# Kernel tuning notes

Measured on AMD Instinct MI355X. Metric: run time of the kernel, lower is better.

Reference implementation:

```python
import jax, jax.numpy as jnp
import numpy as np

N, E, D, C = 100000, 200000, 32, 8
H = 2 * C * C          # 128, MLP hidden
OUT = 4 * C * C + 4 * C  # 288, MLP output


def setup_inputs() -> dict:
    key = jax.random.key(0)
    ks = jax.random.split(key, 10)
    return {
        "x": jax.random.normal(ks[0], (N, D, C), jnp.float32),
        "edge_index": jax.random.randint(ks[1], (2, E), 0, N, jnp.int64),
        "edge_features_a": jax.random.normal(ks[2], (E, D, C), jnp.float32),
        "edge_features_b": jax.random.normal(ks[3], (E, D, C), jnp.float32),
        "edge_matrices": jax.random.normal(ks[4], (E, D, D), jnp.float32),
        "W1": jax.random.normal(ks[5], (H, H), jnp.float32) / np.sqrt(H),
        "b1": jnp.zeros((H,), jnp.float32),
        "ln_g": jnp.ones((H,), jnp.float32),
        "ln_b": jnp.zeros((H,), jnp.float32),
        "W2": jax.random.normal(ks[6], (H, OUT), jnp.float32) / np.sqrt(H),
        "b2": jnp.zeros((OUT,), jnp.float32),
    }


def _matrix_norm(w):
    # unit Frobenius norm over last two dims (MatrixNormalization, scale=1)
    n = jnp.sqrt(jnp.sum(w * w, axis=(-2, -1), keepdims=True))
    return w / (n + 1e-6)


def reference(x, edge_index, edge_features_a, edge_features_b, edge_matrices,
              W1, b1, ln_g, ln_b, W2, b2):
    c = x.shape[-1]
    x_node_a = x[edge_index[0]]                     # [E, D, C]
    x_node_b = x[edge_index[1]]                     # [E, D, C]

    edge_overlap = jnp.einsum('eij,eic,ejm->ecm', edge_matrices,
                              edge_features_a, edge_features_b)  # [E, C, C]
    node_overlap = jnp.einsum('eij,eic,ejm->ecm', edge_matrices,
                              x_node_a, x_node_b)                # [E, C, C]

    h = jnp.concatenate([edge_overlap.reshape(edge_overlap.shape[0], -1),
                         node_overlap.reshape(node_overlap.shape[0], -1)], axis=-1)
    h = jax.nn.silu(h @ W1 + b1)
    mu = jnp.mean(h, axis=-1, keepdims=True)
    var = jnp.var(h, axis=-1, keepdims=True)
    h = (h - mu) / jnp.sqrt(var + 1e-5) * ln_g + ln_b
    mlp_res = h @ W2 + b2                           # [E, 4C^2 + 4C]

    weights = mlp_res[:, :4 * c * c]
    factors = mlp_res[:, 4 * c * c:]
    ew_a, ew_b, nw_a, nw_b = jnp.split(weights, 4, axis=-1)
    ew_a = _matrix_norm(ew_a.reshape(-1, c, c))
    ew_b = _matrix_norm(ew_b.reshape(-1, c, c))
    nw_a = _matrix_norm(nw_a.reshape(-1, c, c))
    nw_b = _matrix_norm(nw_b.reshape(-1, c, c))

    f_ea = factors[:, None, 0 * c:1 * c]
    f_eb = factors[:, None, 1 * c:2 * c]
    f_na = factors[:, None, 2 * c:3 * c]
    f_nb = factors[:, None, 3 * c:4 * c]

    x_edge_a = (f_ea * (edge_features_a @ ew_a) + f_na * (x_node_a @ nw_a)) / 2
    x_edge_b = (f_eb * (edge_features_b @ ew_b) + f_nb * (x_node_b @ nw_b)) / 2
    return (x_edge_a, x_edge_b)
```

## Files before the change

### kernel.cpp

```cpp
#include <hip/hip_runtime.h>
#include <hip/hip_fp16.h>

typedef _Float16 f16;
typedef _Float16 half8 __attribute__((ext_vector_type(8)));
typedef _Float16 half4 __attribute__((ext_vector_type(4)));
typedef float f32x4 __attribute__((ext_vector_type(4)));

static __device__ __forceinline__ void fence_lds(){
  asm volatile("s_waitcnt lgkmcnt(0)" ::: "memory");
  __builtin_amdgcn_sched_barrier(0);
}

__global__ void k0_convert(const float* __restrict__ W1, const float* __restrict__ W2,
                           f16* __restrict__ W1T, f16* __restrict__ W2T){
  int o = blockIdx.x*256 + threadIdx.x;
  if (o < 128*128){
    int j = o >> 7, i = o & 127;
    W1T[o] = (f16)W1[i*128 + j];
  } else {
    int o2 = o - 128*128;
    int n = o2 >> 7, i = o2 & 127;
    W2T[o2] = (f16)W2[i*288 + n];
  }
}

struct ERegs { f32x4 a, b, xa, xb, m0, m1, m2, m3; };

static __device__ __forceinline__ ERegs load_edge(
    const float* __restrict__ x, const int* __restrict__ eidx,
    const float* __restrict__ efa, const float* __restrict__ efb,
    const float* __restrict__ em, int e, int E, int l){
  ERegs r;
  const size_t eb = (size_t)e * 256;
  const int ia = eidx[e], ib = eidx[E + e];
  r.a  = *(const f32x4*)(efa + eb + l*4);
  r.b  = *(const f32x4*)(efb + eb + l*4);
  r.xa = *(const f32x4*)(x + (size_t)ia*256 + l*4);
  r.xb = *(const f32x4*)(x + (size_t)ib*256 + l*4);
  const size_t mb = (size_t)e * 1024;
  r.m0 = *(const f32x4*)(em + mb +   0 + l*4);
  r.m1 = *(const f32x4*)(em + mb + 256 + l*4);
  r.m2 = *(const f32x4*)(em + mb + 512 + l*4);
  r.m3 = *(const f32x4*)(em + mb + 768 + l*4);
  return r;
}

__global__ __launch_bounds__(256, 3) void k_fused(
    const float* __restrict__ x, const int* __restrict__ eidx,
    const float* __restrict__ efa, const float* __restrict__ efb,
    const float* __restrict__ em,
    const f16* __restrict__ W1T, const f16* __restrict__ W2T,
    const float* __restrict__ b1, const float* __restrict__ lng,
    const float* __restrict__ lnb, const float* __restrict__ b2,
    float* __restrict__ outA, float* outB, int E)
{
  __shared__ f16 sWk[17024];

  const int tid = threadIdx.x;
  const int l = tid & 63, w = tid >> 6, q = l >> 4, n16 = l & 15;
  const int e0 = blockIdx.x * 16;

  f16*   sH0   = sWk + 12800;
  f16*   sH1   = sWk + 9344;
  float* sStat = (float*)sWk;
  float* sR    = (float*)sWk;

  f16* Mb   = sWk + w*3200;
  f16* AXT  = Mb + 1280;
  f16* BXT  = AXT + 640;
  f16* MBXT = BXT + 640;

  half4 hA[4], hXa[4], hB[4], hXb[4];

  ERegs cur = load_edge(x, eidx, efa, efb, em, e0 + w*4, E, l);
  #pragma unroll
  for (int i = 0; i < 4; ++i){
    const int le = w*4 + i;
    ERegs nxt;
    if (i < 3) nxt = load_edge(x, eidx, efa, efb, em, e0 + le + 1, E, l);

    {
      int d = l >> 1, cb = (l & 1)*4;
      half4 ta, txa, tb, txb;
      #pragma unroll
      for (int j = 0; j < 4; ++j){
        int c = cb + j;
        f16 va  = (f16)cur.a[j],  vxa = (f16)cur.xa[j];
        f16 vb  = (f16)cur.b[j],  vxb = (f16)cur.xb[j];
        AXT[c*40 + d]     = va;   AXT[(8+c)*40 + d] = vxa;
        BXT[c*40 + d]     = vb;   BXT[(8+c)*40 + d] = vxb;
        ta[j] = va; txa[j] = vxa; tb[j] = vb; txb[j] = vxb;
      }
      hA[i] = ta; hXa[i] = txa; hB[i] = tb; hXb[i] = txb;
      int r0 = l >> 3, c0 = (l & 7)*4;
      f16* p0 = Mb + ( 0 + r0)*40 + c0;
      p0[0]=(f16)cur.m0[0]; p0[1]=(f16)cur.m0[1]; p0[2]=(f16)cur.m0[2]; p0[3]=(f16)cur.m0[3];
      f16* p1 = Mb + ( 8 + r0)*40 + c0;
      p1[0]=(f16)cur.m1[0]; p1[1]=(f16)cur.m1[1]; p1[2]=(f16)cur.m1[2]; p1[3]=(f16)cur.m1[3];
      f16* p2 = Mb + (16 + r0)*40 + c0;
      p2[0]=(f16)cur.m2[0]; p2[1]=(f16)cur.m2[1]; p2[2]=(f16)cur.m2[2]; p2[3]=(f16)cur.m2[3];
      f16* p3 = Mb + (24 + r0)*40 + c0;
      p3[0]=(f16)cur.m3[0]; p3[1]=(f16)cur.m3[1]; p3[2]=(f16)cur.m3[2]; p3[3]=(f16)cur.m3[3];
    }
    fence_lds();

    half8 bF  = *(half8*)(BXT + n16*40 + q*8);
    half8 aF0 = *(half8*)(Mb  + n16*40      + q*8);
    half8 aF1 = *(half8*)(Mb  + (16+n16)*40 + q*8);
    f32x4 z = {0.f,0.f,0.f,0.f};
    f32x4 d0 = __builtin_amdgcn_mfma_f32_16x16x32_f16(aF0, bF, z, 0,0,0);
    f32x4 d1 = __builtin_amdgcn_mfma_f32_16x16x32_f16(aF1, bF, z, 0,0,0);
    {
      f16* p0 = MBXT + n16*40 + q*4;
      p0[0]=(f16)d0[0]; p0[1]=(f16)d0[1]; p0[2]=(f16)d0[2]; p0[3]=(f16)d0[3];
      f16* p1 = MBXT + n16*40 + 16 + q*4;
      p1[0]=(f16)d1[0]; p1[1]=(f16)d1[1]; p1[2]=(f16)d1[2]; p1[3]=(f16)d1[3];
    }
    fence_lds();

    half8 aF2 = *(half8*)(AXT  + n16*40 + q*8);
    half8 bF2 = *(half8*)(MBXT + n16*40 + q*8);
    f32x4 d2 = __builtin_amdgcn_mfma_f32_16x16x32_f16(aF2, bF2, z, 0,0,0);

    if (q < 2 && n16 < 8){
      #pragma unroll
      for (int j=0;j<4;++j){
        int ch = 4*q + j;
        sH0[le*128 + ((ch ^ (le & 7))*8) + n16] = (f16)d2[j];
      }
    }
    if (q >= 2 && n16 >= 8){
      #pragma unroll
      for (int j=0;j<4;++j){
        int ch = 8 + 4*(q-2) + j;
        sH0[le*128 + ((ch ^ (le & 7))*8) + (n16-8)] = (f16)d2[j];
      }
    }
    if (i < 3) cur = nxt;
    fence_lds();
  }
  __syncthreads();

  f32x4 acc[2] = {{0,0,0,0},{0,0,0,0}};
  #pragma unroll
  for (int ks = 0; ks < 4; ++ks){
    half8 aF = *(const half8*)(sH0 + n16*128 + (((ks*4 + q) ^ (n16 & 7))*8));
    #pragma unroll
    for (int c2 = 0; c2 < 2; ++c2){
      int ct = 2*w + c2;
      half8 bF = *(const half8*)(W1T + (size_t)(ct*16 + n16)*128 + ks*32 + q*8);
      acc[c2] = __builtin_amdgcn_mfma_f32_16x16x32_f16(aF, bF, acc[c2], 0,0,0);
    }
  }
  float sv[2][4];
  #pragma unroll
  for (int c2=0;c2<2;++c2)
    #pragma unroll
    for (int j=0;j<4;++j){
      int col = (2*w + c2)*16 + n16;
      float v = acc[c2][j] + b1[col];
      sv[c2][j] = v / (1.f + __expf(-v));
    }
  #pragma unroll
  for (int j=0;j<4;++j){
    float s  = sv[0][j] + sv[1][j];
    float sq = sv[0][j]*sv[0][j] + sv[1][j]*sv[1][j];
    #pragma unroll
    for (int m=1;m<16;m<<=1){ s += __shfl_xor(s, m, 64); sq += __shfl_xor(sq, m, 64); }
    if (n16 == 0){ sStat[(w*16 + 4*q + j)*2] = s; sStat[(w*16 + 4*q + j)*2 + 1] = sq; }
  }
  __syncthreads();
  float mu[4], rs[4];
  #pragma unroll
  for (int j=0;j<4;++j){
    int row = 4*q + j;
    float s=0.f, sq=0.f;
    #pragma unroll
    for (int w2=0;w2<4;++w2){ s += sStat[(w2*16+row)*2]; sq += sStat[(w2*16+row)*2+1]; }
    float m_ = s * (1.f/128.f);
    mu[j] = m_;
    rs[j] = rsqrtf(sq * (1.f/128.f) - m_*m_ + 1e-5f);
  }
  #pragma unroll
  for (int c2=0;c2<2;++c2)
    #pragma unroll
    for (int j=0;j<4;++j){
      int col = (2*w + c2)*16 + n16;
      int row = 4*q + j;
      float hn = (sv[c2][j] - mu[j])*rs[j]*lng[col] + lnb[col];
      sH1[row*128 + (((col>>3) ^ (row&7))*8) + (col&7)] = (f16)hn;
    }
  __syncthreads();

  f32x4 acc2[5] = {{0,0,0,0},{0,0,0,0},{0,0,0,0},{0,0,0,0},{0,0,0,0}};
  #pragma unroll
  for (int ks=0;ks<4;++ks){
    half8 aF = *(const half8*)(sH1 + n16*128 + (((ks*4 + q) ^ (n16 & 7))*8));
    #pragma unroll
    for (int t=0;t<5;++t){
      int ct = w + 4*t;
      if (ct < 18){
        half8 bF = *(const half8*)(W2T + (size_t)(ct*16 + n16)*128 + ks*32 + q*8);
        acc2[t] = __builtin_amdgcn_mfma_f32_16x16x32_f16(aF, bF, acc2[t], 0,0,0);
      }
    }
  }
  #pragma unroll
  for (int t=0;t<5;++t){
    int ct = w + 4*t;
    if (ct < 18){
      #pragma unroll
      for (int j=0;j<4;++j){
        int col = ct*16 + n16, row = 4*q + j;
        sR[row*292 + col] = acc2[t][j] + b2[col];
      }
    }
  }
  __syncthreads();

  f16*   pw    = sWk + 9344 + w*1920;
  f16*   LHSst = pw;
  f16*   RT    = pw + 1280;
  float* sO    = (float*)pw;

  f32x4 w4v[4]; float ssq[4];
  #pragma unroll
  for (int i=0;i<4;++i){
    w4v[i] = *(const f32x4*)(sR + (w*4+i)*292 + l*4);
    ssq[i] = w4v[i][0]*w4v[i][0] + w4v[i][1]*w4v[i][1]
           + w4v[i][2]*w4v[i][2] + w4v[i][3]*w4v[i][3];
  }
  #pragma unroll
  for (int m=1;m<16;m<<=1){
    #pragma unroll
    for (int i=0;i<4;++i) ssq[i] += __shfl_xor(ssq[i], m, 64);
  }
  float rn[4];
  #pragma unroll
  for (int i=0;i<4;++i) rn[i] = 1.f / (sqrtf(ssq[i]) + 1e-6f);

  #pragma unroll
  for (int i = 0; i < 4; ++i){
    const int le = w*4 + i;
    const int e  = e0 + le;
    {
      uint32_t* z32 = (uint32_t*)RT;
      z32[l] = 0u; z32[l+64] = 0u; z32[l+128] = 0u; z32[l+192] = 0u; z32[l+256] = 0u;
    }
    const int mm = l >> 4;
    const int kk = n16 >> 1;
    #pragma unroll
    for (int j=0;j<4;++j){
      int c = (l & 1)*4 + j;
      float f = sR[le*292 + 256 + mm*8 + c];
      f16 val = (f16)(w4v[i][j] * rn[i] * f * 0.5f);
      int nOut = c + (mm & 1)*8;
      int rk   = kk + ((mm & 1) << 4) + ((mm >> 1) << 3);
      RT[nOut*40 + rk] = val;
    }
    {
      int d = l >> 1, cb = (l & 1)*4;
      *(half4*)(LHSst + d*40 + cb)      = hA[i];
      *(half4*)(LHSst + d*40 + 8 + cb)  = hXa[i];
      *(half4*)(LHSst + d*40 + 16 + cb) = hB[i];
      *(half4*)(LHSst + d*40 + 24 + cb) = hXb[i];
    }
    fence_lds();
    half8 bF  = *(const half8*)(RT + n16*40 + q*8);
    half8 aF0 = *(const half8*)(LHSst + n16*40 + q*8);
    half8 aF1 = *(const half8*)(LHSst + (16 + n16)*40 + q*8);
    fence_lds();
    f32x4 z = {0.f,0.f,0.f,0.f};
    f32x4 Dv0 = __builtin_amdgcn_mfma_f32_16x16x32_f16(aF0, bF, z, 0,0,0);
    f32x4 Dv1 = __builtin_amdgcn_mfma_f32_16x16x32_f16(aF1, bF, z, 0,0,0);
    #pragma unroll
    for (int j=0;j<4;++j){
      sO[(      4*q + j)*17 + n16] = Dv0[j];
      sO[(16 +  4*q + j)*17 + n16] = Dv1[j];
    }
    fence_lds();
    {
      const size_t eb = (size_t)e * 256;
      int d = l >> 1, cb = (l & 1)*4;
      f32x4 va, vb;
      #pragma unroll
      for (int j=0;j<4;++j){
        va[j] = sO[d*17 + cb + j];
        vb[j] = sO[d*17 + 8 + cb + j];
      }
      *(f32x4*)(outA + eb + l*4) = va;
      *(f32x4*)(outB + eb + l*4) = vb;
    }
    fence_lds();
  }
}

extern "C" void kernel_launch(void* const* d_in, const int* in_sizes, int n_in,
                              void* d_out, int out_size, void* d_ws, size_t ws_size,
                              hipStream_t stream) {
  const float* x   = (const float*)d_in[0];
  const int*   ei  = (const int*)  d_in[1];
  const float* efa = (const float*)d_in[2];
  const float* efb = (const float*)d_in[3];
  const float* em  = (const float*)d_in[4];
  const float* W1  = (const float*)d_in[5];
  const float* b1  = (const float*)d_in[6];
  const float* lng = (const float*)d_in[7];
  const float* lnb = (const float*)d_in[8];
  const float* W2  = (const float*)d_in[9];
  const float* b2  = (const float*)d_in[10];
  const int E = in_sizes[1] / 2;

  float* outA = (float*)d_out;
  float* outB = outA + (size_t)E*256;
  f16* W1T = (f16*)d_ws;
  f16* W2T = W1T + 128*128;

  k0_convert<<<208, 256, 0, stream>>>(W1, W2, W1T, W2T);
  k_fused<<<E/16, 256, 0, stream>>>(x, ei, efa, efb, em, W1T, W2T,
                                    b1, lng, lnb, b2, outA, outB, E);
}
```

Baseline: 503.7 us.

## Make each wave process its own four edges end-to-end without block barriers

Restructures the fused kernel so every wave owns four edges and runs both MLP GEMMs for them independently, using a private LDS arena and wave-local fences instead of block-wide __syncthreads. Each wave now computes all 8 W1 column tiles and all 18 W2 column tiles on a 16-row MFMA tile where only 4 rows hold real data. This removes cross-wave synchronization and shared statistics, at the cost of roughly four times more MFMA work and more W1/W2 fragment loads per wave.

New measurement: 839.2 us. 66.6% more time.

```diff
diff --git a/kernel.cpp b/kernel.cpp
--- a/kernel.cpp
+++ b/kernel.cpp
@@ -45,39 +45,41 @@
   return r;
 }
 
-__global__ __launch_bounds__(256, 3) void k_fused(
+__global__ __launch_bounds__(256, 3) void k_wave(
     const float* __restrict__ x, const int* __restrict__ eidx,
     const float* __restrict__ efa, const float* __restrict__ efb,
     const float* __restrict__ em,
     const f16* __restrict__ W1T, const f16* __restrict__ W2T,
     const float* __restrict__ b1, const float* __restrict__ lng,
     const float* __restrict__ lnb, const float* __restrict__ b2,
-    float* __restrict__ outA, float* outB, int E)
+    float* __restrict__ outA, float* __restrict__ outB, int E)
 {
-  __shared__ f16 sWk[17024];
+  __shared__ f16 sArena[4*4800];
 
   const int tid = threadIdx.x;
-  const int l = tid & 63, w = tid >> 6, q = l >> 4, n16 = l & 15;
-  const int e0 = blockIdx.x * 16;
-
-  f16*   sH0   = sWk + 12800;
-  f16*   sH1   = sWk + 9344;
-  float* sStat = (float*)sWk;
-  float* sR    = (float*)sWk;
-
-  f16* Mb   = sWk + w*3200;
-  f16* AXT  = Mb + 1280;
-  f16* BXT  = AXT + 640;
-  f16* MBXT = BXT + 640;
+  const int l = tid & 63, w = tid >> 6;
+  const int q = l >> 4, n16 = l & 15;
+  const int e0 = blockIdx.x * 16 + w * 4;
+
+  f16* sWk = sArena + w*4800;
+
+  f16*   Mb    = sWk;
+  f16*   AXT   = Mb + 1280;
+  f16*   BXT   = AXT + 640;
+  f16*   MBXT  = BXT + 640;
+  float* sRw   = (float*)sWk;
+  f16*   LHSst = sWk + 2336;
+  f16*   RT    = sWk + 3616;
+  float* sO    = (float*)(sWk + 2336);
+  f16*   sH    = sWk + 4256;
 
   half4 hA[4], hXa[4], hB[4], hXb[4];
 
-  ERegs cur = load_edge(x, eidx, efa, efb, em, e0 + w*4, E, l);
+  ERegs cur = load_edge(x, eidx, efa, efb, em, e0, E, l);
   #pragma unroll
   for (int i = 0; i < 4; ++i){
-    const int le = w*4 + i;
     ERegs nxt;
-    if (i < 3) nxt = load_edge(x, eidx, efa, efb, em, e0 + le + 1, E, l);
+    if (i < 3) nxt = load_edge(x, eidx, efa, efb, em, e0 + i + 1, E, l);
 
     {
       int d = l >> 1, cb = (l & 1)*4;
@@ -124,109 +126,95 @@
 
     if (q < 2 && n16 < 8){
       #pragma unroll
-      for (int j=0;j<4;++j){
-        int ch = 4*q + j;
-        sH0[le*128 + ((ch ^ (le & 7))*8) + n16] = (f16)d2[j];
+      for (int j=0;j<4;++j) sH[i*136 + (4*q+j)*8 + n16] = (f16)d2[j];
+    }
+    if (q >= 2 && n16 >= 8){
+      #pragma unroll
+      for (int j=0;j<4;++j) sH[i*136 + 64 + (4*(q-2)+j)*8 + (n16-8)] = (f16)d2[j];
+    }
+    if (i < 3) cur = nxt;
+    fence_lds();
+  }
+
+  half8 aFk[4];
+  #pragma unroll
+  for (int ks=0; ks<4; ++ks)
+    aFk[ks] = *(const half8*)(sH + (n16&3)*136 + ks*32 + q*8);
+
+  float sv[8][4];
+  float sAcc[4]  = {0.f,0.f,0.f,0.f};
+  float sqAcc[4] = {0.f,0.f,0.f,0.f};
+  #pragma unroll
+  for (int ct=0; ct<8; ++ct){
+    f32x4 a1 = {0.f,0.f,0.f,0.f};
+    #pragma unroll
+    for (int ks=0; ks<4; ++ks){
+      half8 bF = *(const half8*)(W1T + (ct*16 + n16)*128 + ks*32 + q*8);
+      a1 = __builtin_amdgcn_mfma_f32_16x16x32_f16(aFk[ks], bF, a1, 0,0,0);
+    }
+    float bb = b1[ct*16 + n16];
+    #pragma unroll
+    for (int j=0; j<4; ++j){
+      float v = a1[j] + bb;
+      float s = v / (1.f + __expf(-v));
+      sv[ct][j] = s;
+      sAcc[j] += s; sqAcc[j] += s*s;
+    }
+  }
+  #pragma unroll
+  for (int m=1; m<16; m<<=1){
+    #pragma unroll
+    for (int j=0; j<4; ++j){
+      sAcc[j]  += __shfl_xor(sAcc[j],  m, 64);
+      sqAcc[j] += __shfl_xor(sqAcc[j], m, 64);
+    }
+  }
+  float mu[4], rs[4];
+  #pragma unroll
+  for (int j=0; j<4; ++j){
+    float m_ = sAcc[j] * (1.f/128.f);
+    mu[j] = m_;
+    rs[j] = rsqrtf(sqAcc[j] * (1.f/128.f) - m_*m_ + 1e-5f);
+  }
+  fence_lds();
+  #pragma unroll
+  for (int ct=0; ct<8; ++ct){
+    if ((ct & 3) == q){
+      float g = lng[ct*16 + n16], bb = lnb[ct*16 + n16];
+      #pragma unroll
+      for (int j=0; j<4; ++j){
+        float hn = (sv[ct][j] - mu[j])*rs[j]*g + bb;
+        sH[j*136 + ct*16 + n16] = (f16)hn;
       }
     }
-    if (q >= 2 && n16 >= 8){
-      #pragma unroll
-      for (int j=0;j<4;++j){
-        int ch = 8 + 4*(q-2) + j;
-        sH0[le*128 + ((ch ^ (le & 7))*8) + (n16-8)] = (f16)d2[j];
-      }
-    }
-    if (i < 3) cur = nxt;
-    fence_lds();
-  }
-  __syncthreads();
-
-  f32x4 acc[2] = {{0,0,0,0},{0,0,0,0}};
-  #pragma unroll
-  for (int ks = 0; ks < 4; ++ks){
-    half8 aF = *(const half8*)(sH0 + n16*128 + (((ks*4 + q) ^ (n16 & 7))*8));
-    #pragma unroll
-    for (int c2 = 0; c2 < 2; ++c2){
-      int ct = 2*w + c2;
-      half8 bF = *(const half8*)(W1T + (size_t)(ct*16 + n16)*128 + ks*32 + q*8);
-      acc[c2] = __builtin_amdgcn_mfma_f32_16x16x32_f16(aF, bF, acc[c2], 0,0,0);
-    }
-  }
-  float sv[2][4];
-  #pragma unroll
-  for (int c2=0;c2<2;++c2)
-    #pragma unroll
-    for (int j=0;j<4;++j){
-      int col = (2*w + c2)*16 + n16;
-      float v = acc[c2][j] + b1[col];
-      sv[c2][j] = v / (1.f + __expf(-v));
-    }
-  #pragma unroll
-  for (int j=0;j<4;++j){
-    float s  = sv[0][j] + sv[1][j];
-    float sq = sv[0][j]*sv[0][j] + sv[1][j]*sv[1][j];
-    #pragma unroll
-    for (int m=1;m<16;m<<=1){ s += __shfl_xor(s, m, 64); sq += __shfl_xor(sq, m, 64); }
-    if (n16 == 0){ sStat[(w*16 + 4*q + j)*2] = s; sStat[(w*16 + 4*q + j)*2 + 1] = sq; }
-  }
-  __syncthreads();
-  float mu[4], rs[4];
-  #pragma unroll
-  for (int j=0;j<4;++j){
-    int row = 4*q + j;
-    float s=0.f, sq=0.f;
-    #pragma unroll
-    for (int w2=0;w2<4;++w2){ s += sStat[(w2*16+row)*2]; sq += sStat[(w2*16+row)*2+1]; }
-    float m_ = s * (1.f/128.f);
-    mu[j] = m_;
-    rs[j] = rsqrtf(sq * (1.f/128.f) - m_*m_ + 1e-5f);
-  }
-  #pragma unroll
-  for (int c2=0;c2<2;++c2)
-    #pragma unroll
-    for (int j=0;j<4;++j){
-      int col = (2*w + c2)*16 + n16;
-      int row = 4*q + j;
-      float hn = (sv[c2][j] - mu[j])*rs[j]*lng[col] + lnb[col];
-      sH1[row*128 + (((col>>3) ^ (row&7))*8) + (col&7)] = (f16)hn;
-    }
-  __syncthreads();
-
-  f32x4 acc2[5] = {{0,0,0,0},{0,0,0,0},{0,0,0,0},{0,0,0,0},{0,0,0,0}};
-  #pragma unroll
-  for (int ks=0;ks<4;++ks){
-    half8 aF = *(const half8*)(sH1 + n16*128 + (((ks*4 + q) ^ (n16 & 7))*8));
-    #pragma unroll
-    for (int t=0;t<5;++t){
-      int ct = w + 4*t;
-      if (ct < 18){
-        half8 bF = *(const half8*)(W2T + (size_t)(ct*16 + n16)*128 + ks*32 + q*8);
-        acc2[t] = __builtin_amdgcn_mfma_f32_16x16x32_f16(aF, bF, acc2[t], 0,0,0);
-      }
-    }
-  }
-  #pragma unroll
-  for (int t=0;t<5;++t){
-    int ct = w + 4*t;
-    if (ct < 18){
-      #pragma unroll
-      for (int j=0;j<4;++j){
-        int col = ct*16 + n16, row = 4*q + j;
-        sR[row*292 + col] = acc2[t][j] + b2[col];
-      }
-    }
-  }
-  __syncthreads();
-
-  f16*   pw    = sWk + 9344 + w*1920;
-  f16*   LHSst = pw;
-  f16*   RT    = pw + 1280;
-  float* sO    = (float*)pw;
+  }
+  fence_lds();
+
+  half8 aFh[4];
+  #pragma unroll
+  for (int ks=0; ks<4; ++ks)
+    aFh[ks] = *(const half8*)(sH + (n16&3)*136 + ks*32 + q*8);
+  #pragma unroll
+  for (int ct=0; ct<18; ++ct){
+    f32x4 a2 = {0.f,0.f,0.f,0.f};
+    #pragma unroll
+    for (int ks=0; ks<4; ++ks){
+      half8 bF = *(const half8*)(W2T + (ct*16 + n16)*128 + ks*32 + q*8);
+      a2 = __builtin_amdgcn_mfma_f32_16x16x32_f16(aFh[ks], bF, a2, 0,0,0);
+    }
+    if ((ct & 3) == q){
+      float bb = b2[ct*16 + n16];
+      #pragma unroll
+      for (int j=0; j<4; ++j)
+        sRw[j*292 + ct*16 + n16] = a2[j] + bb;
+    }
+  }
+  fence_lds();
 
   f32x4 w4v[4]; float ssq[4];
   #pragma unroll
   for (int i=0;i<4;++i){
-    w4v[i] = *(const f32x4*)(sR + (w*4+i)*292 + l*4);
+    w4v[i] = *(const f32x4*)(sRw + i*292 + l*4);
     ssq[i] = w4v[i][0]*w4v[i][0] + w4v[i][1]*w4v[i][1]
            + w4v[i][2]*w4v[i][2] + w4v[i][3]*w4v[i][3];
   }
@@ -241,8 +229,7 @@
 
   #pragma unroll
   for (int i = 0; i < 4; ++i){
-    const int le = w*4 + i;
-    const int e  = e0 + le;
+    const int e = e0 + i;
     {
       uint32_t* z32 = (uint32_t*)RT;
       z32[l] = 0u; z32[l+64] = 0u; z32[l+128] = 0u; z32[l+192] = 0u; z32[l+256] = 0u;
@@ -252,7 +239,7 @@
     #pragma unroll
     for (int j=0;j<4;++j){
       int c = (l & 1)*4 + j;
-      float f = sR[le*292 + 256 + mm*8 + c];
+      float f = sRw[i*292 + 256 + mm*8 + c];
       f16 val = (f16)(w4v[i][j] * rn[i] * f * 0.5f);
       int nOut = c + (mm & 1)*8;
       int rk   = kk + ((mm & 1) << 4) + ((mm >> 1) << 3);
@@ -317,6 +304,6 @@
   f16* W2T = W1T + 128*128;
 
   k0_convert<<<208, 256, 0, stream>>>(W1, W2, W1T, W2T);
-  k_fused<<<E/16, 256, 0, stream>>>(x, ei, efa, efb, em, W1T, W2T,
-                                    b1, lng, lnb, b2, outA, outB, E);
-}
+  k_wave<<<E/16, 256, 0, stream>>>(x, ei, efa, efb, em, W1T, W2T,
+                                   b1, lng, lnb, b2, outA, outB, E);
+}
```
